# Optimization experiments

Measured on AMD Instinct MI355X. Metric: run time of the kernel, lower is better.

The kernel has to match this reference:

```python
import jax, jax.numpy as jnp
import numpy as np

N_NODES = 50000
N_EDGES = 300000
D = 256


def setup_inputs() -> dict:
    key = jax.random.key(0)
    k1, k2, k3, k4, k5 = jax.random.split(key, 5)
    edge_feat = jax.random.normal(k1, (N_EDGES, D), dtype=jnp.float32)
    node_feat = jax.random.normal(k2, (N_NODES, D), dtype=jnp.float32)
    src_idx = jax.random.randint(k3, (N_EDGES,), 0, N_NODES, dtype=jnp.int32)
    tgt_idx = jax.random.randint(k4, (N_EDGES,), 0, N_NODES, dtype=jnp.int32)
    W = jax.random.normal(k5, (3 * D, D), dtype=jnp.float32) * (1.0 / np.sqrt(3 * D))
    b = jnp.zeros((D,), dtype=jnp.float32)
    return {"edge_feat": edge_feat, "node_feat": node_feat,
            "src_idx": src_idx, "tgt_idx": tgt_idx, "W": W, "b": b}


def reference(edge_feat, node_feat, src_idx, tgt_idx, W, b):
    # broadcast_node_to_edges: gather node states for SOURCE and TARGET tags
    src = jnp.take(node_feat, src_idx, axis=0)   # [E, D]
    tgt = jnp.take(node_feat, tgt_idx, axis=0)   # [E, D]
    # NextStateFromConcat: concat edge input + node inputs, then Dense+relu
    x = jnp.concatenate([edge_feat, src, tgt], axis=-1)  # [E, 3D]
    return jax.nn.relu(x @ W + b)                        # [E, D]
```

## Files before the change

kernel.cpp:

```cpp
#include <hip/hip_runtime.h>
#include <hip/hip_bf16.h>

typedef __attribute__((ext_vector_type(8))) short short8;
typedef __attribute__((ext_vector_type(4))) float floatx4;

#define D_DIM 256
#define K_DIM 768
#define TILE 128
#define APAD 40

__device__ __forceinline__ short f2bf(float x) {
    union { float f; unsigned u; } a; a.f = x;
    unsigned r = a.u + 0x7fffu + ((a.u >> 16) & 1u);
    return (short)(r >> 16);
}

__global__ __launch_bounds__(256) void wt_kernel(const float* __restrict__ W,
                                                 short* __restrict__ Wt) {
    __shared__ float tile[32][33];
    const int k0 = blockIdx.x * 32, n0 = blockIdx.y * 32;
    const int tx = threadIdx.x & 31, ty = threadIdx.x >> 5;
#pragma unroll
    for (int i = 0; i < 32; i += 8)
        tile[ty + i][tx] = W[(size_t)(k0 + ty + i) * D_DIM + n0 + tx];
    __syncthreads();
#pragma unroll
    for (int i = 0; i < 32; i += 8)
        Wt[(size_t)(n0 + ty + i) * K_DIM + k0 + tx] = f2bf(tile[tx][ty + i]);
}

__global__ __launch_bounds__(256, 3) void edge_gemm(
    const float* __restrict__ edge, const float* __restrict__ node,
    const int* __restrict__ src, const int* __restrict__ tgt,
    const short* __restrict__ Wt, const float* __restrict__ bias,
    float* __restrict__ out, int E)
{
    __shared__ short As[TILE][APAD];
    __shared__ short Bs[TILE][APAD];
    __shared__ int sidx[TILE], tidx[TILE];

    const int tid = threadIdx.x;
    const int m0 = blockIdx.y * TILE;
    const int n0 = blockIdx.x * TILE;

    if (tid < TILE) {
        int r = m0 + tid; if (r >= E) r = E - 1;
        sidx[tid] = src[r];
        tidx[tid] = tgt[r];
    }
    __syncthreads();

    const int srow = tid >> 1;
    const int half = tid & 1;
    int rs = m0 + srow; if (rs >= E) rs = E - 1;
    const float* ab0 = edge + (size_t)rs * D_DIM + half * 16;
    const float* ab1 = node + (size_t)sidx[srow] * D_DIM + half * 16;
    const float* ab2 = node + (size_t)tidx[srow] * D_DIM + half * 16;
    const short* wb  = Wt + (size_t)(n0 + srow) * K_DIM + half * 16;
    short* aw = &As[srow][half * 16];
    short* bw = &Bs[srow][half * 16];

    const int lane = tid & 63;
    const int wm = ((tid >> 7) & 1) * 64;
    const int wn = ((tid >> 6) & 1) * 64;
    const int fr = lane & 15;
    const int kq = (lane >> 4) * 8;

    floatx4 acc[4][4] = {};

    const float* abases[3] = { ab0, ab1, ab2 };

#pragma unroll
    for (int seg = 0; seg < 3; ++seg) {
        const float* ab = abases[seg];
        const short* wbs = wb + seg * D_DIM;
        for (int it = 0; it < 8; ++it) {
            const float4* ap = (const float4*)(ab + it * 32);
            float4 f0 = ap[0], f1 = ap[1], f2 = ap[2], f3 = ap[3];
            const short8* wp = (const short8*)(wbs + it * 32);
            short8 w0 = wp[0], w1 = wp[1];

            __syncthreads();

            union { short8 v; short s[8]; } u0, u1;
            u0.s[0] = f2bf(f0.x); u0.s[1] = f2bf(f0.y); u0.s[2] = f2bf(f0.z); u0.s[3] = f2bf(f0.w);
            u0.s[4] = f2bf(f1.x); u0.s[5] = f2bf(f1.y); u0.s[6] = f2bf(f1.z); u0.s[7] = f2bf(f1.w);
            u1.s[0] = f2bf(f2.x); u1.s[1] = f2bf(f2.y); u1.s[2] = f2bf(f2.z); u1.s[3] = f2bf(f2.w);
            u1.s[4] = f2bf(f3.x); u1.s[5] = f2bf(f3.y); u1.s[6] = f2bf(f3.z); u1.s[7] = f2bf(f3.w);
            *(short8*)aw = u0.v;       *((short8*)aw + 1) = u1.v;
            *(short8*)bw = w0;         *((short8*)bw + 1) = w1;

            __syncthreads();

            short8 afr[4], bfr[4];
#pragma unroll
            for (int i = 0; i < 4; ++i) afr[i] = *(const short8*)&As[wm + i * 16 + fr][kq];
#pragma unroll
            for (int j = 0; j < 4; ++j) bfr[j] = *(const short8*)&Bs[wn + j * 16 + fr][kq];
#pragma unroll
            for (int i = 0; i < 4; ++i)
#pragma unroll
                for (int j = 0; j < 4; ++j)
                    acc[i][j] = __builtin_amdgcn_mfma_f32_16x16x32_bf16(
                        afr[i], bfr[j], acc[i][j], 0, 0, 0);
        }
    }

    float bv[4];
#pragma unroll
    for (int j = 0; j < 4; ++j) bv[j] = bias[n0 + wn + j * 16 + fr];
    const int rq = (lane >> 4) * 4;
#pragma unroll
    for (int i = 0; i < 4; ++i) {
        const int rbase = m0 + wm + i * 16 + rq;
#pragma unroll
        for (int j = 0; j < 4; ++j) {
            const int c = n0 + wn + j * 16 + fr;
#pragma unroll
            for (int r = 0; r < 4; ++r) {
                const int rr = rbase + r;
                if (rr < E) {
                    float v = acc[i][j][r] + bv[j];
                    out[(size_t)rr * D_DIM + c] = v > 0.f ? v : 0.f;
                }
            }
        }
    }
}

extern "C" void kernel_launch(void* const* d_in, const int* in_sizes, int n_in,
                              void* d_out, int out_size, void* d_ws, size_t ws_size,
                              hipStream_t stream) {
    const float* edge = (const float*)d_in[0];
    const float* node = (const float*)d_in[1];
    const int*   srcI = (const int*)d_in[2];
    const int*   tgtI = (const int*)d_in[3];
    const float* W    = (const float*)d_in[4];
    const float* bias = (const float*)d_in[5];
    float* out = (float*)d_out;
    const int E = in_sizes[2];
    short* Wt = (short*)d_ws;

    dim3 tgrid(K_DIM / 32, D_DIM / 32);
    wt_kernel<<<tgrid, dim3(256), 0, stream>>>(W, Wt);

    dim3 ggrid(D_DIM / TILE, (E + TILE - 1) / TILE);
    edge_gemm<<<ggrid, dim3(256), 0, stream>>>(edge, node, srcI, tgtI, Wt, bias, out, E);
}
```

Before: 789.9 us.

## Use full-N 64-row tiles with double-buffered LDS and register prefetch

Each block now covers 64 edge rows across all 256 output columns, so every gathered A row is loaded and converted to bf16 once rather than once per N-tile. The K loop is software-pipelined: it double-buffers A and B in shared memory, prefetches the next tile's global loads into registers while the current tile is computed, and needs one barrier per step instead of two. In exchange each block streams the whole Wt slice (256x32 per step), which raises B traffic per output row. LDS use also grows, which may lower occupancy under launch_bounds(256,3).

```diff
diff --git a/kernel.cpp b/kernel.cpp
--- a/kernel.cpp
+++ b/kernel.cpp
@@ -6,8 +6,10 @@
 
 #define D_DIM 256
 #define K_DIM 768
-#define TILE 128
-#define APAD 40
+#define BM 64
+#define BK 32
+#define PAD 40
+#define NSTEP 24
 
 __device__ __forceinline__ short f2bf(float x) {
     union { float f; unsigned u; } a; a.f = x;
@@ -35,87 +37,105 @@
     const short* __restrict__ Wt, const float* __restrict__ bias,
     float* __restrict__ out, int E)
 {
-    __shared__ short As[TILE][APAD];
-    __shared__ short Bs[TILE][APAD];
-    __shared__ int sidx[TILE], tidx[TILE];
+    __shared__ short As[2][BM][PAD];
+    __shared__ short Bs[2][D_DIM][PAD];
 
     const int tid = threadIdx.x;
-    const int m0 = blockIdx.y * TILE;
-    const int n0 = blockIdx.x * TILE;
+    const int m0 = blockIdx.x * BM;
 
-    if (tid < TILE) {
-        int r = m0 + tid; if (r >= E) r = E - 1;
-        sidx[tid] = src[r];
-        tidx[tid] = tgt[r];
-    }
-    __syncthreads();
-
-    const int srow = tid >> 1;
-    const int half = tid & 1;
-    int rs = m0 + srow; if (rs >= E) rs = E - 1;
-    const float* ab0 = edge + (size_t)rs * D_DIM + half * 16;
-    const float* ab1 = node + (size_t)sidx[srow] * D_DIM + half * 16;
-    const float* ab2 = node + (size_t)tidx[srow] * D_DIM + half * 16;
-    const short* wb  = Wt + (size_t)(n0 + srow) * K_DIM + half * 16;
-    short* aw = &As[srow][half * 16];
-    short* bw = &Bs[srow][half * 16];
+    const int arow = tid >> 2;
+    const int achk = (tid & 3) * 8;
+    int rs = m0 + arow; if (rs >= E) rs = E - 1;
+    const int si = src[rs], ti = tgt[rs];
+    const float* a0 = edge + (size_t)rs * D_DIM + achk;
+    const float* a1 = node + (size_t)si * D_DIM + achk;
+    const float* a2 = node + (size_t)ti * D_DIM + achk;
+    const short* wrow = Wt + (size_t)tid * K_DIM;
 
     const int lane = tid & 63;
-    const int wm = ((tid >> 7) & 1) * 64;
-    const int wn = ((tid >> 6) & 1) * 64;
+    const int wv = tid >> 6;
     const int fr = lane & 15;
     const int kq = (lane >> 4) * 8;
 
     floatx4 acc[4][4] = {};
 
-    const float* abases[3] = { ab0, ab1, ab2 };
+    float4 pA0, pA1, qA0, qA1;
+    short8 rB0, rB1, rB2, rB3;
 
-#pragma unroll
-    for (int seg = 0; seg < 3; ++seg) {
-        const float* ab = abases[seg];
-        const short* wbs = wb + seg * D_DIM;
-        for (int it = 0; it < 8; ++it) {
-            const float4* ap = (const float4*)(ab + it * 32);
-            float4 f0 = ap[0], f1 = ap[1], f2 = ap[2], f3 = ap[3];
-            const short8* wp = (const short8*)(wbs + it * 32);
-            short8 w0 = wp[0], w1 = wp[1];
+#define LOADA(d0, d1, t) { \
+    const int sg_ = (t) >> 3; \
+    const float* ab_ = sg_ == 0 ? a0 : (sg_ == 1 ? a1 : a2); \
+    const float4* ap_ = (const float4*)(ab_ + ((t) & 7) * BK); \
+    d0 = ap_[0]; d1 = ap_[1]; }
 
-            __syncthreads();
+#define LOADB(t) { \
+    const short8* bp_ = (const short8*)(wrow + (t) * BK); \
+    rB0 = bp_[0]; rB1 = bp_[1]; rB2 = bp_[2]; rB3 = bp_[3]; }
 
-            union { short8 v; short s[8]; } u0, u1;
-            u0.s[0] = f2bf(f0.x); u0.s[1] = f2bf(f0.y); u0.s[2] = f2bf(f0.z); u0.s[3] = f2bf(f0.w);
-            u0.s[4] = f2bf(f1.x); u0.s[5] = f2bf(f1.y); u0.s[6] = f2bf(f1.z); u0.s[7] = f2bf(f1.w);
-            u1.s[0] = f2bf(f2.x); u1.s[1] = f2bf(f2.y); u1.s[2] = f2bf(f2.z); u1.s[3] = f2bf(f2.w);
-            u1.s[4] = f2bf(f3.x); u1.s[5] = f2bf(f3.y); u1.s[6] = f2bf(f3.z); u1.s[7] = f2bf(f3.w);
-            *(short8*)aw = u0.v;       *((short8*)aw + 1) = u1.v;
-            *(short8*)bw = w0;         *((short8*)bw + 1) = w1;
+#define STORE(b, s0, s1) { \
+    union { short8 v; short s[8]; } u_; \
+    u_.s[0] = f2bf(s0.x); u_.s[1] = f2bf(s0.y); u_.s[2] = f2bf(s0.z); u_.s[3] = f2bf(s0.w); \
+    u_.s[4] = f2bf(s1.x); u_.s[5] = f2bf(s1.y); u_.s[6] = f2bf(s1.z); u_.s[7] = f2bf(s1.w); \
+    *(short8*)&As[b][arow][achk] = u_.v; \
+    *(short8*)&Bs[b][tid][0]  = rB0; \
+    *(short8*)&Bs[b][tid][8]  = rB1; \
+    *(short8*)&Bs[b][tid][16] = rB2; \
+    *(short8*)&Bs[b][tid][24] = rB3; }
 
-            __syncthreads();
+#define COMPUTE(b) { \
+    short8 bfr0 = *(const short8*)&Bs[b][wv * 64 +  0 + fr][kq]; \
+    short8 bfr1 = *(const short8*)&Bs[b][wv * 64 + 16 + fr][kq]; \
+    short8 bfr2 = *(const short8*)&Bs[b][wv * 64 + 32 + fr][kq]; \
+    short8 bfr3 = *(const short8*)&Bs[b][wv * 64 + 48 + fr][kq]; \
+    _Pragma("unroll") \
+    for (int i_ = 0; i_ < 4; ++i_) { \
+        short8 afr = *(const short8*)&As[b][i_ * 16 + fr][kq]; \
+        acc[i_][0] = __builtin_amdgcn_mfma_f32_16x16x32_bf16(afr, bfr0, acc[i_][0], 0, 0, 0); \
+        acc[i_][1] = __builtin_amdgcn_mfma_f32_16x16x32_bf16(afr, bfr1, acc[i_][1], 0, 0, 0); \
+        acc[i_][2] = __builtin_amdgcn_mfma_f32_16x16x32_bf16(afr, bfr2, acc[i_][2], 0, 0, 0); \
+        acc[i_][3] = __builtin_amdgcn_mfma_f32_16x16x32_bf16(afr, bfr3, acc[i_][3], 0, 0, 0); \
+    } }
 
-            short8 afr[4], bfr[4];
-#pragma unroll
-            for (int i = 0; i < 4; ++i) afr[i] = *(const short8*)&As[wm + i * 16 + fr][kq];
-#pragma unroll
-            for (int j = 0; j < 4; ++j) bfr[j] = *(const short8*)&Bs[wn + j * 16 + fr][kq];
-#pragma unroll
-            for (int i = 0; i < 4; ++i)
-#pragma unroll
-                for (int j = 0; j < 4; ++j)
-                    acc[i][j] = __builtin_amdgcn_mfma_f32_16x16x32_bf16(
-                        afr[i], bfr[j], acc[i][j], 0, 0, 0);
-        }
+    LOADB(0);
+    LOADA(qA0, qA1, 0);
+    STORE(0, qA0, qA1);
+    LOADA(qA0, qA1, 1);
+    __syncthreads();
+
+#pragma unroll 1
+    for (int t = 0; t < 22; t += 2) {
+        LOADB(t + 1);
+        LOADA(pA0, pA1, t + 2);
+        COMPUTE(0);
+        STORE(1, qA0, qA1);
+        __syncthreads();
+        LOADB(t + 2);
+        LOADA(qA0, qA1, t + 3);
+        COMPUTE(1);
+        STORE(0, pA0, pA1);
+        __syncthreads();
     }
+    LOADB(23);
+    COMPUTE(0);
+    STORE(1, qA0, qA1);
+    __syncthreads();
+    COMPUTE(1);
+
+#undef LOADA
+#undef LOADB
+#undef STORE
+#undef COMPUTE
 
     float bv[4];
 #pragma unroll
-    for (int j = 0; j < 4; ++j) bv[j] = bias[n0 + wn + j * 16 + fr];
+    for (int j = 0; j < 4; ++j) bv[j] = bias[wv * 64 + j * 16 + fr];
     const int rq = (lane >> 4) * 4;
 #pragma unroll
     for (int i = 0; i < 4; ++i) {
-        const int rbase = m0 + wm + i * 16 + rq;
+        const int rbase = m0 + i * 16 + rq;
 #pragma unroll
         for (int j = 0; j < 4; ++j) {
-            const int c = n0 + wn + j * 16 + fr;
+            const int c = wv * 64 + j * 16 + fr;
 #pragma unroll
             for (int r = 0; r < 4; ++r) {
                 const int rr = rbase + r;
@@ -144,6 +164,6 @@
     dim3 tgrid(K_DIM / 32, D_DIM / 32);
     wt_kernel<<<tgrid, dim3(256), 0, stream>>>(W, Wt);
 
-    dim3 ggrid(D_DIM / TILE, (E + TILE - 1) / TILE);
+    dim3 ggrid((E + BM - 1) / BM);
     edge_gemm<<<ggrid, dim3(256), 0, stream>>>(edge, node, srcI, tgtI, Wt, bias, out, E);
 }
```

New measurement: 813.6 us. +3.0%, slower.
